# Kernel optimization log

Hardware: AMD Instinct MI355X
Metric: run time of the kernel (lower is better)

Reference implementation:

```python
import jax, jax.numpy as jnp
import numpy as np

N_DRUG = 20000
N_DIS = 20000
E = 300000
D_IN = 128
D_OUT = 128
W_SCALE = 0.05  # ~xavier-ish scale so leaky_relu/softmax stay well-conditioned


def setup_inputs() -> dict:
    key = jax.random.key(0)
    ks = jax.random.split(key, 17)
    f32 = jnp.float32
    inp = {
        'feat_drug': jax.random.normal(ks[0], (N_DRUG, D_IN), dtype=f32),
        'feat_disease': jax.random.normal(ks[1], (N_DIS, D_IN), dtype=f32),
        'W_ind': jax.random.normal(ks[2], (D_IN, D_OUT), dtype=f32) * W_SCALE,
        'b_ind': jax.random.normal(ks[3], (D_OUT,), dtype=f32) * W_SCALE,
        'a_ind': jax.random.normal(ks[4], (2 * D_OUT,), dtype=f32) * W_SCALE,
        'W_rev': jax.random.normal(ks[5], (D_IN, D_OUT), dtype=f32) * W_SCALE,
        'b_rev': jax.random.normal(ks[6], (D_OUT,), dtype=f32) * W_SCALE,
        'a_rev': jax.random.normal(ks[7], (2 * D_OUT,), dtype=f32) * W_SCALE,
        'W_dd': jax.random.normal(ks[8], (D_IN, D_OUT), dtype=f32) * W_SCALE,
        'b_dd': jax.random.normal(ks[9], (D_OUT,), dtype=f32) * W_SCALE,
        'a_dd': jax.random.normal(ks[10], (2 * D_OUT,), dtype=f32) * W_SCALE,
        'src_ind': jax.random.randint(ks[11], (E,), 0, N_DRUG, dtype=jnp.int32),
        'dst_ind': jax.random.randint(ks[12], (E,), 0, N_DIS, dtype=jnp.int32),
        'src_rev': jax.random.randint(ks[13], (E,), 0, N_DIS, dtype=jnp.int32),
        'dst_rev': jax.random.randint(ks[14], (E,), 0, N_DRUG, dtype=jnp.int32),
        'src_dd': jax.random.randint(ks[15], (E,), 0, N_DIS, dtype=jnp.int32),
        'dst_dd': jax.random.randint(ks[16], (E,), 0, N_DIS, dtype=jnp.int32),
    }
    return inp


def segment_softmax(e, seg, num_segments):
    # numerically stable softmax over variable-degree neighborhoods (dst segments)
    m = jax.ops.segment_max(e, seg, num_segments=num_segments)
    p = jnp.exp(e - m[seg])
    s = jax.ops.segment_sum(p, seg, num_segments=num_segments)
    return p / s[seg]


def _etype_agg(Wh_src, Wh_dst_key, a, src, dst, n_dst):
    # attn_fc(cat([Wh_src[src], Wh_dst_key[dst]])) decomposed into per-node
    # scalar projections, then gathered per edge (same math, far less traffic)
    d = Wh_src.shape[1]
    el = Wh_src @ a[:d]        # [n_src]
    er = Wh_dst_key @ a[d:]    # [n_dst]
    e = jax.nn.leaky_relu(el[src] + er[dst])          # [E], slope 0.01 as in torch
    alpha = segment_softmax(e, dst, n_dst)            # per-dst softmax (DGL mailbox)
    msg = alpha[:, None] * Wh_src[src]                # [E, d]
    return jax.ops.segment_sum(msg, dst, num_segments=n_dst)


def reference(feat_drug, feat_disease, W_ind, b_ind, a_ind, W_rev, b_rev, a_rev,
              W_dd, b_dd, a_dd, src_ind, dst_ind, src_rev, dst_rev, src_dd, dst_dd):
    # per-etype linear on source node type
    Wh_ind = feat_drug @ W_ind + b_ind       # drug nodes, etype 'indication'
    Wh_rev = feat_disease @ W_rev + b_rev    # disease nodes, etype 'rev_indication'
    Wh_dd = feat_disease @ W_dd + b_dd       # disease nodes, etype 'disease_disease'
    n_drug = feat_drug.shape[0]
    n_dis = feat_disease.shape[0]
    # etype 'indication' (drug->disease): dst key is Wh_rev_indication
    h_dis_ind = _etype_agg(Wh_ind, Wh_rev, a_ind, src_ind, dst_ind, n_dis)
    # etype 'rev_indication' (disease->drug): dst key is Wh_indication
    h_drug = _etype_agg(Wh_rev, Wh_ind, a_rev, src_rev, dst_rev, n_drug)
    # etype 'disease_disease' (homotypic): both keys Wh_dd
    h_dis_dd = _etype_agg(Wh_dd, Wh_dd, a_dd, src_dd, dst_dd, n_dis)
    # multi_update_all(..., 'sum'): sum per-etype reductions per dst node type
    h_disease = h_dis_ind + h_dis_dd
    return h_drug, h_disease
```

## Files before the change

kernel.cpp:

```cpp
#include <hip/hip_runtime.h>
#include <hip/hip_bf16.h>

typedef __hip_bfloat16 bf16;
typedef __attribute__((ext_vector_type(8))) short bf16x8;
typedef __attribute__((ext_vector_type(4))) float f32x4;

#define N_NODE 20000
#define D      128
#define NEDGE  300000
#define NROW   (3 * N_NODE)
#define NBIN   ((NROW + 255) >> 8)
#define NB3    220
#define CHUNK  4096
#define GBE    ((N_NODE + 63) / 64)
#define GEMMB  (3 * GBE)
#define WT_LD  132

__device__ __forceinline__ short f2bs(float x) {
    bf16 h = __float2bfloat16(x);
    short s; __builtin_memcpy(&s, &h, 2); return s;
}

union SharedA {
    short Wt[D * WT_LD];
    int   h[NBIN];
};

__global__ __launch_bounds__(256) void gemm_and_count(
    const float* __restrict__ feat_drug, const float* __restrict__ feat_dis,
    const float* __restrict__ W_ind, const float* __restrict__ b_ind,
    const float* __restrict__ a_ind,
    const float* __restrict__ W_rev, const float* __restrict__ b_rev,
    const float* __restrict__ a_rev,
    const float* __restrict__ W_dd, const float* __restrict__ b_dd,
    const float* __restrict__ a_dd,
    const int* __restrict__ dst_rev, const int* __restrict__ dst_ind,
    const int* __restrict__ dst_dd,
    bf16* __restrict__ Wh_all, float* __restrict__ el_all,
    float* __restrict__ er_all, int* __restrict__ bin_part) {
    __shared__ SharedA su;
    const int tid = threadIdx.x;

    if (blockIdx.x >= GEMMB) {
        const int blk = blockIdx.x - GEMMB;
        for (int i = tid; i < NBIN; i += 256) su.h[i] = 0;
        __syncthreads();
        const int base = blk * CHUNK;
        const int lim = min(base + CHUNK, 3 * NEDGE);
        for (int i = base + tid; i < lim; i += 256) {
            const int t = (i >= 2 * NEDGE) ? 2 : (i >= NEDGE ? 1 : 0);
            const int e = i - t * NEDGE;
            const int d = (t == 0 ? dst_rev : (t == 1 ? dst_ind : dst_dd))[e];
            atomicAdd(&su.h[(t * N_NODE + d) >> 8], 1);
        }
        __syncthreads();
        for (int i = tid; i < NBIN; i += 256)
            bin_part[blk * NBIN + i] = su.h[i];
        return;
    }

    const int t  = blockIdx.x / GBE;
    const int mb = blockIdx.x - t * GBE;

    const float *feat, *W, *bias, *va, *vb;
    float *el_o, *er_o;
    if (t == 0)      { feat = feat_dis;  W = W_rev; bias = b_rev; va = a_rev; vb = a_ind + D; el_o = el_all;              er_o = er_all + N_NODE; }
    else if (t == 1) { feat = feat_drug; W = W_ind; bias = b_ind; va = a_ind; vb = a_rev + D; el_o = el_all + N_NODE;     er_o = er_all; }
    else             { feat = feat_dis;  W = W_dd;  bias = b_dd;  va = a_dd;  vb = a_dd + D;  el_o = el_all + 2 * N_NODE; er_o = er_all + 2 * N_NODE; }
    bf16* wh_o = Wh_all + (size_t)t * N_NODE * D;

    for (int i = tid * 4; i < D * D; i += 1024) {
        const float4 wv = *(const float4*)(W + i);
        const int k = i >> 7, n = i & (D - 1);
        su.Wt[(n + 0) * WT_LD + k] = f2bs(wv.x);
        su.Wt[(n + 1) * WT_LD + k] = f2bs(wv.y);
        su.Wt[(n + 2) * WT_LD + k] = f2bs(wv.z);
        su.Wt[(n + 3) * WT_LD + k] = f2bs(wv.w);
    }
    __syncthreads();

    const int wave = tid >> 6, lane = tid & 63;
    const int q = lane >> 4, nn = lane & 15;
    const int row0 = mb * 64 + wave * 16;
    const int arow = min(row0 + nn, N_NODE - 1);

    f32x4 acc[8];
#pragma unroll
    for (int nt = 0; nt < 8; ++nt) acc[nt] = (f32x4){0.f, 0.f, 0.f, 0.f};

#pragma unroll
    for (int ks = 0; ks < 4; ++ks) {
        const float* ap = feat + (size_t)arow * D + ks * 32 + q * 8;
        const float4 fa = *(const float4*)ap;
        const float4 fb = *(const float4*)(ap + 4);
        bf16x8 afrag;
        afrag[0] = f2bs(fa.x); afrag[1] = f2bs(fa.y);
        afrag[2] = f2bs(fa.z); afrag[3] = f2bs(fa.w);
        afrag[4] = f2bs(fb.x); afrag[5] = f2bs(fb.y);
        afrag[6] = f2bs(fb.z); afrag[7] = f2bs(fb.w);
#pragma unroll
        for (int nt = 0; nt < 8; ++nt) {
            const bf16x8 bfrag =
                *(const bf16x8*)(&su.Wt[(nt * 16 + nn) * WT_LD + ks * 32 + q * 8]);
            acc[nt] = __builtin_amdgcn_mfma_f32_16x16x32_bf16(afrag, bfrag,
                                                              acc[nt], 0, 0, 0);
        }
    }

    float biasv[8], vav[8], vbv[8];
#pragma unroll
    for (int nt = 0; nt < 8; ++nt) {
        const int col = nt * 16 + nn;
        biasv[nt] = bias[col]; vav[nt] = va[col]; vbv[nt] = vb[col];
    }
    float pel[4] = {0.f, 0.f, 0.f, 0.f};
    float per_[4] = {0.f, 0.f, 0.f, 0.f};
    short* whs = (short*)wh_o;
#pragma unroll
    for (int nt = 0; nt < 8; ++nt) {
#pragma unroll
        for (int r = 0; r < 4; ++r) {
            const float c = acc[nt][r] + biasv[nt];
            const int grow = row0 + q * 4 + r;
            if (grow < N_NODE)
                whs[(size_t)grow * D + nt * 16 + nn] = f2bs(c);
            pel[r] = fmaf(c, vav[nt], pel[r]);
            per_[r] = fmaf(c, vbv[nt], per_[r]);
        }
    }
#pragma unroll
    for (int r = 0; r < 4; ++r) {
#pragma unroll
        for (int mask = 1; mask < 16; mask <<= 1) {
            pel[r]  += __shfl_xor(pel[r],  mask, 64);
            per_[r] += __shfl_xor(per_[r], mask, 64);
        }
        const int grow = row0 + q * 4 + r;
        if (nn == 0 && grow < N_NODE) {
            el_o[grow] = pel[r];
            er_o[grow] = per_[r];
        }
    }
}

__global__ __launch_bounds__(256) void binscat(
    const int* __restrict__ src_rev, const int* __restrict__ dst_rev,
    const int* __restrict__ src_ind, const int* __restrict__ dst_ind,
    const int* __restrict__ src_dd,  const int* __restrict__ dst_dd,
    const int* __restrict__ bin_part, int* __restrict__ bin_base_g,
    int* __restrict__ row_ptr, unsigned* __restrict__ bin_buf) {
    __shared__ int runc[NBIN];
    __shared__ int wsum[4];
    const int blk = blockIdx.x;
    const int tid = threadIdx.x;
    const int lane = tid & 63, wave = tid >> 6;

    int tot = 0, pre = 0;
    if (tid < NBIN) {
        for (int j = 0; j < NB3; ++j) {
            const int c = bin_part[j * NBIN + tid];
            tot += c;
            pre += (j < blk) ? c : 0;
        }
    }
    int v = (tid < NBIN) ? tot : 0;
    const int orig = v;
#pragma unroll
    for (int off = 1; off < 64; off <<= 1) {
        int t = __shfl_up(v, off, 64);
        if (lane >= off) v += t;
    }
    if (lane == 63) wsum[wave] = v;
    __syncthreads();
    if (tid == 0) {
        int a = 0;
#pragma unroll
        for (int w = 0; w < 4; ++w) { int t = wsum[w]; wsum[w] = a; a += t; }
    }
    __syncthreads();
    const int excl = wsum[wave] + v - orig;
    if (tid < NBIN) runc[tid] = excl + pre;
    if (blk == 0) {
        if (tid < NBIN) bin_base_g[tid] = excl;
        if (tid == 0) { bin_base_g[NBIN] = 3 * NEDGE; row_ptr[NROW] = 3 * NEDGE; }
    }
    __syncthreads();

    const int base = blk * CHUNK;
    const int lim = min(base + CHUNK, 3 * NEDGE);
    for (int i = base + tid; i < lim; i += 256) {
        const int t = (i >= 2 * NEDGE) ? 2 : (i >= NEDGE ? 1 : 0);
        const int e = i - t * NEDGE;
        const int sl = (t == 0 ? src_rev : (t == 1 ? src_ind : src_dd))[e];
        const int dl = (t == 0 ? dst_rev : (t == 1 ? dst_ind : dst_dd))[e];
        const int row = t * N_NODE + dl;
        const int slot = atomicAdd(&runc[row >> 8], 1);
        bin_buf[slot] = ((unsigned)row << 16) | (unsigned)(t * N_NODE + sl);
    }
}

__global__ __launch_bounds__(256) void binsort(
    const int* __restrict__ bin_base, const unsigned* __restrict__ bin_buf,
    int* __restrict__ row_ptr, unsigned short* __restrict__ edge_src16) {
    __shared__ int rowcnt[256];
    __shared__ int rankc[256];
    __shared__ int wsum[4];
    const int b = blockIdx.x;
    const int tid = threadIdx.x;
    const int beg = bin_base[b], end = bin_base[b + 1];
    rowcnt[tid] = 0;
    __syncthreads();
    for (int i = beg + tid; i < end; i += 256)
        atomicAdd(&rowcnt[(bin_buf[i] >> 16) & 255], 1);
    __syncthreads();
    const int lane = tid & 63, wave = tid >> 6;
    int v = rowcnt[tid];
    const int orig = v;
#pragma unroll
    for (int off = 1; off < 64; off <<= 1) {
        int t = __shfl_up(v, off, 64);
        if (lane >= off) v += t;
    }
    if (lane == 63) wsum[wave] = v;
    __syncthreads();
    if (tid == 0) {
        int a = 0;
#pragma unroll
        for (int w = 0; w < 4; ++w) { int t = wsum[w]; wsum[w] = a; a += t; }
    }
    __syncthreads();
    const int excl = wsum[wave] + v - orig;
    const int row = b * 256 + tid;
    if (row < NROW) row_ptr[row] = beg + excl;
    rankc[tid] = beg + excl;
    __syncthreads();
    for (int i = beg + tid; i < end; i += 256) {
        const unsigned u = bin_buf[i];
        const int slot = atomicAdd(&rankc[(u >> 16) & 255], 1);
        edge_src16[slot] = (unsigned short)(u & 0xFFFFu);
    }
}

__device__ __forceinline__ void process_chunk(
    int msrc, float mpe, int m, float inv, int lane,
    const bf16* __restrict__ Wh_all, float& a0, float& a1) {
    int t = 0;
    for (; t + 4 <= m; t += 4) {
        const int s0 = __shfl(msrc, t,     64);
        const int s1 = __shfl(msrc, t + 1, 64);
        const int s2 = __shfl(msrc, t + 2, 64);
        const int s3 = __shfl(msrc, t + 3, 64);
        const float c0 = __shfl(mpe, t,     64) * inv;
        const float c1 = __shfl(mpe, t + 1, 64) * inv;
        const float c2 = __shfl(mpe, t + 2, 64) * inv;
        const float c3 = __shfl(mpe, t + 3, 64) * inv;
        const unsigned u0 = ((const unsigned*)(Wh_all + (size_t)s0 * D))[lane];
        const unsigned u1 = ((const unsigned*)(Wh_all + (size_t)s1 * D))[lane];
        const unsigned u2 = ((const unsigned*)(Wh_all + (size_t)s2 * D))[lane];
        const unsigned u3 = ((const unsigned*)(Wh_all + (size_t)s3 * D))[lane];
        a0 = fmaf(c0, __uint_as_float(u0 << 16), a0);
        a1 = fmaf(c0, __uint_as_float(u0 & 0xFFFF0000u), a1);
        a0 = fmaf(c1, __uint_as_float(u1 << 16), a0);
        a1 = fmaf(c1, __uint_as_float(u1 & 0xFFFF0000u), a1);
        a0 = fmaf(c2, __uint_as_float(u2 << 16), a0);
        a1 = fmaf(c2, __uint_as_float(u2 & 0xFFFF0000u), a1);
        a0 = fmaf(c3, __uint_as_float(u3 << 16), a0);
        a1 = fmaf(c3, __uint_as_float(u3 & 0xFFFF0000u), a1);
    }
    for (; t < m; ++t) {
        const int s0 = __shfl(msrc, t, 64);
        const float c0 = __shfl(mpe, t, 64) * inv;
        const unsigned u0 = ((const unsigned*)(Wh_all + (size_t)s0 * D))[lane];
        a0 = fmaf(c0, __uint_as_float(u0 << 16), a0);
        a1 = fmaf(c0, __uint_as_float(u0 & 0xFFFF0000u), a1);
    }
}

__device__ __forceinline__ void do_range(
    const unsigned short* __restrict__ edge_src16,
    const float* __restrict__ el_all, float er_r,
    const bf16* __restrict__ Wh_all,
    int beg, int end, int lane, float& a0, float& a1) {
    if (end <= beg) return;
    const int deg = end - beg;
    const int m0 = min(deg, 64);

    int msrc0 = 0; float mpe0 = 0.f;
    if (lane < m0) {
        msrc0 = edge_src16[beg + lane];
        float v = el_all[msrc0] + er_r;
        v = v > 0.f ? v : 0.01f * v;
        mpe0 = __expf(v);
    }
    float ssum = mpe0;
    for (int base = beg + 64; base < end; base += 64) {
        const int m = min(end - base, 64);
        if (lane < m) {
            const int sr = edge_src16[base + lane];
            float v = el_all[sr] + er_r;
            v = v > 0.f ? v : 0.01f * v;
            ssum += __expf(v);
        }
    }
#pragma unroll
    for (int off = 32; off > 0; off >>= 1) ssum += __shfl_down(ssum, off, 64);
    const float inv = 1.0f / __shfl(ssum, 0, 64);

    process_chunk(msrc0, mpe0, m0, inv, lane, Wh_all, a0, a1);
    for (int base = beg + 64; base < end; base += 64) {
        const int m = min(end - base, 64);
        int msrc = 0; float mpe = 0.f;
        if (lane < m) {
            msrc = edge_src16[base + lane];
            float v = el_all[msrc] + er_r;
            v = v > 0.f ? v : 0.01f * v;
            mpe = __expf(v);
        }
        process_chunk(msrc, mpe, m, inv, lane, Wh_all, a0, a1);
    }
}

__global__ __launch_bounds__(256) void gather_all(
    const int* __restrict__ row_ptr, const unsigned short* __restrict__ edge_src16,
    const float* __restrict__ el_all, const float* __restrict__ er_all,
    const bf16* __restrict__ Wh_all, float* __restrict__ out) {
    const int w = blockIdx.x * (blockDim.x >> 6) + (threadIdx.x >> 6);
    const int lane = threadIdx.x & 63;
    if (w >= 2 * N_NODE) return;

    float a0 = 0.f, a1 = 0.f;
    do_range(edge_src16, el_all, er_all[w], Wh_all,
             row_ptr[w], row_ptr[w + 1], lane, a0, a1);
    if (w >= N_NODE) {
        const int r = w + N_NODE;
        do_range(edge_src16, el_all, er_all[r], Wh_all,
                 row_ptr[r], row_ptr[r + 1], lane, a0, a1);
    }
    ((float2*)(out + (size_t)w * D))[lane] = make_float2(a0, a1);
}

extern "C" void kernel_launch(void* const* d_in, const int* in_sizes, int n_in,
                              void* d_out, int out_size, void* d_ws, size_t ws_size,
                              hipStream_t stream) {
    const float* feat_drug    = (const float*)d_in[0];
    const float* feat_disease = (const float*)d_in[1];
    const float* W_ind = (const float*)d_in[2];
    const float* b_ind = (const float*)d_in[3];
    const float* a_ind = (const float*)d_in[4];
    const float* W_rev = (const float*)d_in[5];
    const float* b_rev = (const float*)d_in[6];
    const float* a_rev = (const float*)d_in[7];
    const float* W_dd  = (const float*)d_in[8];
    const float* b_dd  = (const float*)d_in[9];
    const float* a_dd  = (const float*)d_in[10];
    const int* src_ind = (const int*)d_in[11];
    const int* dst_ind = (const int*)d_in[12];
    const int* src_rev = (const int*)d_in[13];
    const int* dst_rev = (const int*)d_in[14];
    const int* src_dd  = (const int*)d_in[15];
    const int* dst_dd  = (const int*)d_in[16];
    float* out = (float*)d_out;
    (void)in_sizes; (void)n_in; (void)out_size; (void)ws_size;

    char* w = (char*)d_ws;
    bf16*  Wh_all   = (bf16*)w;
    float* el_all   = (float*)(w + 15360000);
    float* er_all   = (float*)(w + 15600000);
    int*   row_ptr  = (int*)(w + 15840000);
    int*   bin_base = (int*)(w + 16080032);
    int*   bin_part = (int*)(w + 16081056);
    unsigned* bin_buf = (unsigned*)(w + 16287872);
    unsigned short* edge_src16 = (unsigned short*)(w + 19887872);

    const int gb = (2 * N_NODE + 3) / 4;

    gemm_and_count<<<GEMMB + NB3, 256, 0, stream>>>(
        feat_drug, feat_disease, W_ind, b_ind, a_ind,
        W_rev, b_rev, a_rev, W_dd, b_dd, a_dd,
        dst_rev, dst_ind, dst_dd, Wh_all, el_all, er_all, bin_part);

    binscat<<<NB3, 256, 0, stream>>>(src_rev, dst_rev, src_ind, dst_ind,
                                     src_dd, dst_dd, bin_part, bin_base,
                                     row_ptr, bin_buf);

    binsort<<<NBIN, 256, 0, stream>>>(bin_base, bin_buf, row_ptr, edge_src16);

    gather_all<<<gb, 256, 0, stream>>>(row_ptr, edge_src16, el_all, er_all,
                                       Wh_all, out);
}
```

Before: 181.3 us.

## Merge indication and disease-disease edges into one CSR row per disease node

The CSR is rebuilt with 2*N rows instead of 3*N. Edges of the indication and disease_disease types that share a destination disease now fall into one row, and the source id (>= 2N) tells which etype an edge belongs to. The gather kernel keeps two softmax sums per row and applies the matching normalizer to each edge, so a disease node is handled in one pass over one row instead of two ranges. This cuts row_ptr size, bins and per-warp passes, and improves warp utilisation for low-degree rows, at the cost of extra per-edge selects.

```diff
diff --git a/kernel.cpp b/kernel.cpp
--- a/kernel.cpp
+++ b/kernel.cpp
@@ -8,8 +8,8 @@
 #define N_NODE 20000
 #define D      128
 #define NEDGE  300000
-#define NROW   (3 * N_NODE)
-#define NBIN   ((NROW + 255) >> 8)
+#define NROW2  (2 * N_NODE)
+#define NBIN   ((NROW2 + 255) >> 8)
 #define NB3    220
 #define CHUNK  4096
 #define GBE    ((N_NODE + 63) / 64)
@@ -51,7 +51,8 @@
             const int t = (i >= 2 * NEDGE) ? 2 : (i >= NEDGE ? 1 : 0);
             const int e = i - t * NEDGE;
             const int d = (t == 0 ? dst_rev : (t == 1 ? dst_ind : dst_dd))[e];
-            atomicAdd(&su.h[(t * N_NODE + d) >> 8], 1);
+            const int row = (t == 0) ? d : (N_NODE + d);
+            atomicAdd(&su.h[row >> 8], 1);
         }
         __syncthreads();
         for (int i = tid; i < NBIN; i += 256)
@@ -182,7 +183,7 @@
     if (tid < NBIN) runc[tid] = excl + pre;
     if (blk == 0) {
         if (tid < NBIN) bin_base_g[tid] = excl;
-        if (tid == 0) { bin_base_g[NBIN] = 3 * NEDGE; row_ptr[NROW] = 3 * NEDGE; }
+        if (tid == 0) { bin_base_g[NBIN] = 3 * NEDGE; row_ptr[NROW2] = 3 * NEDGE; }
     }
     __syncthreads();
 
@@ -193,7 +194,7 @@
         const int e = i - t * NEDGE;
         const int sl = (t == 0 ? src_rev : (t == 1 ? src_ind : src_dd))[e];
         const int dl = (t == 0 ? dst_rev : (t == 1 ? dst_ind : dst_dd))[e];
-        const int row = t * N_NODE + dl;
+        const int row = (t == 0) ? dl : (N_NODE + dl);
         const int slot = atomicAdd(&runc[row >> 8], 1);
         bin_buf[slot] = ((unsigned)row << 16) | (unsigned)(t * N_NODE + sl);
     }
@@ -231,7 +232,7 @@
     __syncthreads();
     const int excl = wsum[wave] + v - orig;
     const int row = b * 256 + tid;
-    if (row < NROW) row_ptr[row] = beg + excl;
+    if (row < NROW2) row_ptr[row] = beg + excl;
     rankc[tid] = beg + excl;
     __syncthreads();
     for (int i = beg + tid; i < end; i += 256) {
@@ -242,7 +243,7 @@
 }
 
 __device__ __forceinline__ void process_chunk(
-    int msrc, float mpe, int m, float inv, int lane,
+    int msrc, float mc, int m, int lane,
     const bf16* __restrict__ Wh_all, float& a0, float& a1) {
     int t = 0;
     for (; t + 4 <= m; t += 4) {
@@ -250,10 +251,10 @@
         const int s1 = __shfl(msrc, t + 1, 64);
         const int s2 = __shfl(msrc, t + 2, 64);
         const int s3 = __shfl(msrc, t + 3, 64);
-        const float c0 = __shfl(mpe, t,     64) * inv;
-        const float c1 = __shfl(mpe, t + 1, 64) * inv;
-        const float c2 = __shfl(mpe, t + 2, 64) * inv;
-        const float c3 = __shfl(mpe, t + 3, 64) * inv;
+        const float c0 = __shfl(mc, t,     64);
+        const float c1 = __shfl(mc, t + 1, 64);
+        const float c2 = __shfl(mc, t + 2, 64);
+        const float c3 = __shfl(mc, t + 3, 64);
         const unsigned u0 = ((const unsigned*)(Wh_all + (size_t)s0 * D))[lane];
         const unsigned u1 = ((const unsigned*)(Wh_all + (size_t)s1 * D))[lane];
         const unsigned u2 = ((const unsigned*)(Wh_all + (size_t)s2 * D))[lane];
@@ -269,54 +270,10 @@
     }
     for (; t < m; ++t) {
         const int s0 = __shfl(msrc, t, 64);
-        const float c0 = __shfl(mpe, t, 64) * inv;
+        const float c0 = __shfl(mc, t, 64);
         const unsigned u0 = ((const unsigned*)(Wh_all + (size_t)s0 * D))[lane];
         a0 = fmaf(c0, __uint_as_float(u0 << 16), a0);
         a1 = fmaf(c0, __uint_as_float(u0 & 0xFFFF0000u), a1);
-    }
-}
-
-__device__ __forceinline__ void do_range(
-    const unsigned short* __restrict__ edge_src16,
-    const float* __restrict__ el_all, float er_r,
-    const bf16* __restrict__ Wh_all,
-    int beg, int end, int lane, float& a0, float& a1) {
-    if (end <= beg) return;
-    const int deg = end - beg;
-    const int m0 = min(deg, 64);
-
-    int msrc0 = 0; float mpe0 = 0.f;
-    if (lane < m0) {
-        msrc0 = edge_src16[beg + lane];
-        float v = el_all[msrc0] + er_r;
-        v = v > 0.f ? v : 0.01f * v;
-        mpe0 = __expf(v);
-    }
-    float ssum = mpe0;
-    for (int base = beg + 64; base < end; base += 64) {
-        const int m = min(end - base, 64);
-        if (lane < m) {
-            const int sr = edge_src16[base + lane];
-            float v = el_all[sr] + er_r;
-            v = v > 0.f ? v : 0.01f * v;
-            ssum += __expf(v);
-        }
-    }
-#pragma unroll
-    for (int off = 32; off > 0; off >>= 1) ssum += __shfl_down(ssum, off, 64);
-    const float inv = 1.0f / __shfl(ssum, 0, 64);
-
-    process_chunk(msrc0, mpe0, m0, inv, lane, Wh_all, a0, a1);
-    for (int base = beg + 64; base < end; base += 64) {
-        const int m = min(end - base, 64);
-        int msrc = 0; float mpe = 0.f;
-        if (lane < m) {
-            msrc = edge_src16[base + lane];
-            float v = el_all[msrc] + er_r;
-            v = v > 0.f ? v : 0.01f * v;
-            mpe = __expf(v);
-        }
-        process_chunk(msrc, mpe, m, inv, lane, Wh_all, a0, a1);
     }
 }
 
@@ -326,15 +283,61 @@
     const bf16* __restrict__ Wh_all, float* __restrict__ out) {
     const int w = blockIdx.x * (blockDim.x >> 6) + (threadIdx.x >> 6);
     const int lane = threadIdx.x & 63;
-    if (w >= 2 * N_NODE) return;
-
+    if (w >= NROW2) return;
+
+    const int beg = row_ptr[w], end = row_ptr[w + 1];
     float a0 = 0.f, a1 = 0.f;
-    do_range(edge_src16, el_all, er_all[w], Wh_all,
-             row_ptr[w], row_ptr[w + 1], lane, a0, a1);
-    if (w >= N_NODE) {
-        const int r = w + N_NODE;
-        do_range(edge_src16, el_all, er_all[r], Wh_all,
-                 row_ptr[r], row_ptr[r + 1], lane, a0, a1);
+    if (end > beg) {
+        const float erA = er_all[w];
+        const float erB = (w >= N_NODE) ? er_all[w + N_NODE] : 0.f;
+        const int m0 = min(end - beg, 64);
+
+        int g0 = 0; float pe0 = 0.f; bool sel0 = false;
+        if (lane < m0) {
+            g0 = edge_src16[beg + lane];
+            sel0 = (g0 >= 2 * N_NODE);
+            float v = el_all[g0] + (sel0 ? erB : erA);
+            v = v > 0.f ? v : 0.01f * v;
+            pe0 = __expf(v);
+        }
+        float sA = sel0 ? 0.f : pe0;
+        float sB = sel0 ? pe0 : 0.f;
+        for (int base = beg + 64; base < end; base += 64) {
+            const int m = min(end - base, 64);
+            if (lane < m) {
+                const int g = edge_src16[base + lane];
+                const bool sel = (g >= 2 * N_NODE);
+                float v = el_all[g] + (sel ? erB : erA);
+                v = v > 0.f ? v : 0.01f * v;
+                const float pe = __expf(v);
+                sA += sel ? 0.f : pe;
+                sB += sel ? pe : 0.f;
+            }
+        }
+#pragma unroll
+        for (int off = 32; off > 0; off >>= 1) {
+            sA += __shfl_down(sA, off, 64);
+            sB += __shfl_down(sB, off, 64);
+        }
+        sA = __shfl(sA, 0, 64);
+        sB = __shfl(sB, 0, 64);
+        const float invA = (sA > 0.f) ? 1.0f / sA : 0.f;
+        const float invB = (sB > 0.f) ? 1.0f / sB : 0.f;
+
+        const float c0 = pe0 * (sel0 ? invB : invA);
+        process_chunk(g0, c0, m0, lane, Wh_all, a0, a1);
+        for (int base = beg + 64; base < end; base += 64) {
+            const int m = min(end - base, 64);
+            int g = 0; float c = 0.f;
+            if (lane < m) {
+                g = edge_src16[base + lane];
+                const bool sel = (g >= 2 * N_NODE);
+                float v = el_all[g] + (sel ? erB : erA);
+                v = v > 0.f ? v : 0.01f * v;
+                c = __expf(v) * (sel ? invB : invA);
+            }
+            process_chunk(g, c, m, lane, Wh_all, a0, a1);
+        }
     }
     ((float2*)(out + (size_t)w * D))[lane] = make_float2(a0, a1);
 }
@@ -367,12 +370,12 @@
     float* el_all   = (float*)(w + 15360000);
     float* er_all   = (float*)(w + 15600000);
     int*   row_ptr  = (int*)(w + 15840000);
-    int*   bin_base = (int*)(w + 16080032);
-    int*   bin_part = (int*)(w + 16081056);
-    unsigned* bin_buf = (unsigned*)(w + 16287872);
-    unsigned short* edge_src16 = (unsigned short*)(w + 19887872);
-
-    const int gb = (2 * N_NODE + 3) / 4;
+    int*   bin_base = (int*)(w + 16000032);
+    int*   bin_part = (int*)(w + 16001056);
+    unsigned* bin_buf = (unsigned*)(w + 16139232);
+    unsigned short* edge_src16 = (unsigned short*)(w + 19739232);
+
+    const int gb = (NROW2 + 3) / 4;
 
     gemm_and_count<<<GEMMB + NB3, 256, 0, stream>>>(
         feat_drug, feat_disease, W_ind, b_ind, a_ind,
```

Measured after the change: 185.8 us. 2.5% more time.
